# Kernel tuning notes

Measured on AMD Instinct MI355X. Metric: run time of the kernel, lower is better.

## Reference

```python
import jax, jax.numpy as jnp
import numpy as np

B, T, D, H = 2, 1024, 1024, 8  # batch, seq, hidden, num_attention_heads


def setup_inputs() -> dict:
    key = jax.random.key(0)
    ks = jax.random.split(key, 7)
    s = 1.0 / np.sqrt(D)
    return {
        "query": jax.random.normal(ks[0], (B, T, D), jnp.float32),
        "key": jax.random.normal(ks[1], (B, T, D), jnp.float32),
        "value": jax.random.normal(ks[2], (B, T, D), jnp.float32),
        "Wq": jax.random.normal(ks[3], (H, D, D), jnp.float32) * s,
        "Wk": jax.random.normal(ks[4], (H, D, D), jnp.float32) * s,
        "Wv": jax.random.normal(ks[5], (D, D), jnp.float32) * s,
        "Wo": jax.random.normal(ks[6], (D, D), jnp.float32) * s,
    }


def reference(query, key, value, Wq, Wk, Wv, Wo):
    b, t, Dm = query.shape
    h = Wq.shape[0]
    d = Dm // h  # head_dim of the inner split
    # Per-outer-head full linear projections: q_i = query @ Wq[i].T  (nn.Linear, bias=False)
    q = jnp.einsum('btd,ied->ibte', query, Wq)   # (i, b, t, D)
    k = jnp.einsum('bsd,ied->ibse', key, Wk)     # (i, b, s, D)
    v = jnp.einsum('bsd,ed->bse', value, Wv)     # shared values (b, s, D)
    # rearrange 'b t (h d) -> b h t d' per outer head i
    q = q.reshape(h, b, t, h, d).transpose(0, 1, 3, 2, 4)  # (i, b, h, t, d)
    k = k.reshape(h, b, t, h, d).transpose(0, 1, 3, 2, 4)  # (i, b, h, s, d)
    v = v.reshape(b, t, h, d).transpose(0, 2, 1, 3)        # (b, h, s, d)
    scale = jnp.sqrt(jnp.asarray(d, jnp.float32))
    scores = jnp.einsum('ibhtd,ibhsd->ibhts', q, k) / scale
    attn = jax.nn.softmax(scores, axis=-1)                 # (i, b, h, t, s)
    head = jnp.einsum('ibhts,bhsd->ibhtd', attn, v)
    # 'b h t d -> b t (h d)' then stack over i and mean
    head = head.transpose(0, 1, 3, 2, 4).reshape(h, b, t, Dm)
    outputs = jnp.mean(head, axis=0) @ Wo.T                # (b, t, D)
    attention = jnp.mean(attn, axis=0)                     # (b, h, t, s)
    return outputs, attention
```

## Files before the change

kernel.cpp:

```cpp
#include <hip/hip_runtime.h>
#include <hip/hip_bf16.h>

typedef _Float16 f16x8 __attribute__((ext_vector_type(8)));
typedef _Float16 f16x4 __attribute__((ext_vector_type(4)));
typedef float f32x4 __attribute__((ext_vector_type(4)));

typedef __attribute__((address_space(1))) void GV;
typedef __attribute__((address_space(3))) void LV;

__device__ inline void async16(void* lds, const void* g) {
    __builtin_amdgcn_global_load_lds((GV*)g, (LV*)lds, 16, 0, 0);
}

__global__ __launch_bounds__(256) void cast_all(
    const float* __restrict__ q, const float* __restrict__ k, const float* __restrict__ v,
    const float* __restrict__ wq, const float* __restrict__ wk,
    const float* __restrict__ wv, const float* __restrict__ wo, _Float16* __restrict__ ws)
{
    const long M1 = 1048576;
    const long tot = 6291456;
    for (long idx = (long)blockIdx.x * 256 + threadIdx.x; idx < tot;
         idx += (long)gridDim.x * 256) {
        const float* src; long local; long doff;
        if (idx < 1572864) {
            int seg = (int)(idx >> 19);
            src = seg == 0 ? q : (seg == 1 ? k : v);
            local = idx & 524287; doff = (long)seg * 2 * M1;
        } else if (idx < 5767168) {
            int seg = (int)((idx - 1572864) >> 21);
            src = seg == 0 ? wq : wk;
            local = (idx - 1572864) & 2097151; doff = (6 + 8 * (long)seg) * M1;
        } else {
            int seg = (int)((idx - 5767168) >> 18);
            src = seg == 0 ? wv : wo;
            local = (idx - 5767168) & 262143; doff = (22 + (long)seg) * M1;
        }
        float4 val = ((const float4*)src)[local];
        f16x4 o;
        o[0] = (_Float16)val.x; o[1] = (_Float16)val.y;
        o[2] = (_Float16)val.z; o[3] = (_Float16)val.w;
        *(f16x4*)&ws[doff + 4 * local] = o;
    }
}

__global__ __launch_bounds__(256) void transpose_v(const _Float16* __restrict__ in,
                                                   _Float16* __restrict__ out) {
    __shared__ _Float16 tile[64][66];
    int b = blockIdx.z;
    long base = (long)b * 1048576;
    int s0 = blockIdx.x * 64, e0 = blockIdx.y * 64;
    int tc = threadIdx.x & 63, tr = threadIdx.x >> 6;
    #pragma unroll
    for (int rr = 0; rr < 64; rr += 4)
        tile[tr + rr][tc] = in[base + (long)(s0 + tr + rr) * 1024 + e0 + tc];
    __syncthreads();
    #pragma unroll
    for (int rr = 0; rr < 64; rr += 4)
        out[base + (long)(e0 + tr + rr) * 1024 + s0 + tc] = tile[tc][tr + rr];
}

template<int RB, int XS, int OMODE>
__global__ __launch_bounds__(256) void gemm_bt(
    const _Float16* __restrict__ A0, const _Float16* __restrict__ B0, void* __restrict__ C0,
    int K, int lda, int ldb, int ldc,
    int az_div, long sa_hi, long sa_lo, long sb,
    int cz_div, long sc_hi, long sc_lo)
{
    __shared__ _Float16 As[2][RB * 32 * 64];
    __shared__ _Float16 Bs[2][128 * 64];
    int bx, by, bz;
    if (XS) {
        int p = blockIdx.x;
        int xcd = p & 7, s = p >> 3;
        int c, within;
        if (s < 256) { c = xcd + 8 * (s >> 6); within = s & 63; }
        else         { c = 32 + (xcd >> 2); within = (xcd & 3) * 16 + (s - 256); }
        bz = c >> 1;
        by = (c & 1) * 8 + (within >> 3);
        bx = within & 7;
    } else { bx = blockIdx.x; by = blockIdx.y; bz = blockIdx.z; }
    int z = bz;
    const _Float16* A = A0 + (long)(z / az_div) * sa_hi + (long)(z % az_div) * sa_lo;
    const _Float16* B = B0 + (long)z * sb;
    long coff = (long)(z / cz_div) * sc_hi + (long)(z % cz_div) * sc_lo;
    int rowbase = by * (RB * 32), colbase = bx * 128;
    int t = threadIdx.x, wave = t >> 6, lane = t & 63;
    int l15 = lane & 15, lg = lane >> 4;
    int srow = t >> 3, scol = (t & 7) * 8;
    int wm = wave >> 1, wn = wave & 1;
    f32x4 acc[RB][4] = {};
    const int nt = K >> 6;

    #pragma unroll
    for (int ii = 0; ii < RB; ii++) {
        int r = srow + ii * 32;
        async16(&As[0][r * 64 + scol], A + (long)(rowbase + r) * lda + scol);
    }
    #pragma unroll
    for (int ii = 0; ii < 4; ii++) {
        int r = srow + ii * 32;
        async16(&Bs[0][r * 64 + scol], B + (long)(colbase + r) * ldb + scol);
    }

    for (int ts = 0; ts < nt; ts++) {
        __syncthreads();
        if (ts + 1 < nt) {
            int k1 = (ts + 1) << 6;
            int p1 = (ts + 1) & 1;
            #pragma unroll
            for (int ii = 0; ii < RB; ii++) {
                int r = srow + ii * 32;
                async16(&As[p1][r * 64 + scol], A + (long)(rowbase + r) * lda + k1 + scol);
            }
            #pragma unroll
            for (int ii = 0; ii < 4; ii++) {
                int r = srow + ii * 32;
                async16(&Bs[p1][r * 64 + scol], B + (long)(colbase + r) * ldb + k1 + scol);
            }
        }
        int pc = ts & 1;
        #pragma unroll
        for (int ks = 0; ks < 2; ks++) {
            f16x8 af[RB], bfr[4];
            #pragma unroll
            for (int m = 0; m < RB; m++)
                af[m] = *(const f16x8*)&As[pc][(wm * (RB * 16) + m * 16 + l15) * 64 + ks * 32 + lg * 8];
            #pragma unroll
            for (int n = 0; n < 4; n++)
                bfr[n] = *(const f16x8*)&Bs[pc][(wn * 64 + n * 16 + l15) * 64 + ks * 32 + lg * 8];
            #pragma unroll
            for (int m = 0; m < RB; m++)
                #pragma unroll
                for (int n = 0; n < 4; n++)
                    acc[m][n] = __builtin_amdgcn_mfma_f32_16x16x32_f16(af[m], bfr[n], acc[m][n], 0, 0, 0);
        }
    }
    #pragma unroll
    for (int m = 0; m < RB; m++) {
        int row = rowbase + wm * (RB * 16) + m * 16 + lg * 4;
        #pragma unroll
        for (int n = 0; n < 4; n++) {
            int col = colbase + wn * 64 + n * 16 + l15;
            #pragma unroll
            for (int r = 0; r < 4; r++) {
                long idx = coff + (long)(row + r) * ldc + col;
                if (OMODE == 1) ((float*)C0)[idx] = acc[m][n][r];
                else ((_Float16*)C0)[idx] = (_Float16)acc[m][n][r];
            }
        }
    }
}

__global__ __launch_bounds__(256, 2) void attn_fused(
    const _Float16* __restrict__ Qbuf, const _Float16* __restrict__ Kbuf,
    float* __restrict__ attn_out, _Float16* __restrict__ Pbar)
{
    __shared__ _Float16 Kc[4][64 * 128];
    __shared__ float red[4][16];
    int id = blockIdx.x;
    int orig = (id & 7) * 128 + (id >> 3);
    int t0 = (orig & 63) * 16;
    int bh = orig >> 6, h = bh & 7, b = bh >> 3;
    int tid = threadIdx.x, wave = tid >> 6, lane = tid & 63;
    int l15 = lane & 15, lg = lane >> 4;
    int sw = wave;
    int brow = sw * 16 + l15;
    const float scale = 0.088388347648318447f;
    float acc[16][4] = {};

    int srow0 = tid >> 4;
    int scolB = (tid & 15) << 4;
    int gcolB = scolB ^ ((srow0 & 7) << 4);
    int ldsoff = tid * 16;
    const char* pkb = (const char*)(Kbuf + (long)b * 1048576 + h * 128)
                      + (long)srow0 * 2048 + gcolB;
    const char* pq = (const char*)(Qbuf + ((long)(b * 1024 + t0 + l15)) * 1024 + h * 128)
                     + lg * 16;
    int swz = (brow & 7) << 4;
    int rdoff[4];
    #pragma unroll
    for (int kk = 0; kk < 4; kk++)
        rdoff[kk] = brow * 256 + ((kk * 64 + lg * 16) ^ swz);

    #pragma unroll
    for (int mp = 0; mp < 3; mp++) {
        char* lb = (char*)Kc[mp] + ldsoff;
        const char* ps = pkb + (long)mp * 131072;
        #pragma unroll
        for (int j = 0; j < 4; j++)
            async16(lb + j * 4096, ps + (long)j * 32768);
    }

    #pragma unroll 1
    for (int i = 0; i < 8; i++) {
        f16x8 aq[4];
        #pragma unroll
        for (int kk = 0; kk < 4; kk++)
            aq[kk] = *(const f16x8*)(pq + kk * 64);
        pq += 4194304;
        float s[16][4];
        float rs[4] = {0.f, 0.f, 0.f, 0.f};
        #pragma unroll
        for (int c = 0; c < 16; c++) {
            int m = i * 16 + c;
            asm volatile("s_waitcnt vmcnt(8) lgkmcnt(0)" ::: "memory");
            __builtin_amdgcn_s_barrier();
            {
                int n = (m + 3) & 127;
                char* lb = (char*)Kc[(c + 3) & 3] + ldsoff;
                const char* ps = pkb + (long)(n >> 4) * 4194304 + (long)(n & 15) * 131072;
                #pragma unroll
                for (int j = 0; j < 4; j++)
                    async16(lb + j * 4096, ps + (long)j * 32768);
            }
            const char* kc = (const char*)Kc[c & 3];
            f32x4 sv = {0.f, 0.f, 0.f, 0.f};
            #pragma unroll
            for (int kk = 0; kk < 4; kk++) {
                f16x8 bk = *(const f16x8*)(kc + rdoff[kk]);
                sv = __builtin_amdgcn_mfma_f32_16x16x32_f16(aq[kk], bk, sv, 0, 0, 0);
            }
            #pragma unroll
            for (int r = 0; r < 4; r++) {
                float e = __expf(sv[r] * scale);
                s[c][r] = e;
                rs[r] += e;
            }
        }
        #pragma unroll
        for (int off = 1; off < 16; off <<= 1)
            #pragma unroll
            for (int r = 0; r < 4; r++) rs[r] += __shfl_xor(rs[r], off, 64);
        if (l15 == 0) {
            #pragma unroll
            for (int r = 0; r < 4; r++) red[wave][lg * 4 + r] = rs[r];
        }
        asm volatile("s_waitcnt lgkmcnt(0)" ::: "memory");
        __builtin_amdgcn_s_barrier();
        #pragma unroll
        for (int r = 0; r < 4; r++) {
            int row = lg * 4 + r;
            float tot = red[0][row] + red[1][row] + red[2][row] + red[3][row];
            float rinv = 0.125f / tot;
            #pragma unroll
            for (int c = 0; c < 16; c++) acc[c][r] += s[c][r] * rinv;
        }
        asm volatile("s_waitcnt lgkmcnt(0)" ::: "memory");
        __builtin_amdgcn_s_barrier();
    }

    long rbase = ((long)(bh * 1024 + t0)) * 1024;
    #pragma unroll
    for (int c = 0; c < 16; c++) {
        int scol = c * 64 + sw * 16 + l15;
        #pragma unroll
        for (int r = 0; r < 4; r++) {
            long idx = rbase + (long)(lg * 4 + r) * 1024 + scol;
            attn_out[idx] = acc[c][r];
            Pbar[idx] = (_Float16)acc[c][r];
        }
    }
}

extern "C" void kernel_launch(void* const* d_in, const int* in_sizes, int n_in,
                              void* d_out, int out_size, void* d_ws, size_t ws_size,
                              hipStream_t stream) {
    const long M1 = 1048576;
    _Float16* ws = (_Float16*)d_ws;
    _Float16* q16  = ws;
    _Float16* wq16 = ws + 6 * M1;
    _Float16* wo16 = ws + 23 * M1;
    _Float16* Qbuf = ws + 24 * M1;
    _Float16* Vbuf = ws + 56 * M1;
    _Float16* Vt   = ws + 58 * M1;
    _Float16* Pb   = ws + 60 * M1;
    _Float16* Hbar = ws + 76 * M1;
    float* out = (float*)d_out;
    float* attn_out = out + 2 * M1;

    cast_all<<<2048, 256, 0, stream>>>(
        (const float*)d_in[0], (const float*)d_in[1], (const float*)d_in[2],
        (const float*)d_in[3], (const float*)d_in[4], (const float*)d_in[5],
        (const float*)d_in[6], ws);

    gemm_bt<4, 1, 0><<<2176, 256, 0, stream>>>(
        q16, wq16, Qbuf, 1024, 1024, 1024, 1024,
         8, 2 * M1, 0,  M1,
         16, 32 * M1, 2 * M1);
    transpose_v<<<dim3(16, 16, 2), 256, 0, stream>>>(Vbuf, Vt);
    attn_fused<<<1024, 256, 0, stream>>>(Qbuf, Qbuf + 16 * M1, attn_out, Pb);
    gemm_bt<2, 0, 0><<<dim3(1, 16, 16), 256, 0, stream>>>(
        Pb, Vt, Hbar, 1024, 1024, 1024, 1024,
         16, 0, M1,  M1 / 8,
         8, M1, 128);
    gemm_bt<2, 0, 1><<<dim3(8, 32, 1), 256, 0, stream>>>(
        Hbar, wo16, out, 1024, 1024, 1024, 1024,
        1, 0, 0, 0, 1, 0, 0);
}
```

Measured before the change: 304.3 us.

## Restructure GEMM staging into a 4-buffer K=32 pipeline with fragment-ordered LDS

The GEMM main loop moves from a double-buffered K=64 tile to a four-slot ring of K=32 tiles with three stages prefetched, synchronised by explicit vmcnt waits and a raw barrier. LDS is laid out in MFMA fragment order, so each lane reads a contiguous 16-byte slot with no bank conflicts, and launch bounds now request two blocks per CU. The aim is to hide global-load latency and cut LDS bank conflicts. In exchange it uses more LDS per block, relies on hand-tuned waitcnt values, and wraps the prefetch index with nt-1, which assumes nt is a power of two.

```diff
diff --git a/kernel.cpp b/kernel.cpp
--- a/kernel.cpp
+++ b/kernel.cpp
@@ -60,14 +60,15 @@
 }
 
 template<int RB, int XS, int OMODE>
-__global__ __launch_bounds__(256) void gemm_bt(
+__global__ __launch_bounds__(256, 2) void gemm_bt(
     const _Float16* __restrict__ A0, const _Float16* __restrict__ B0, void* __restrict__ C0,
     int K, int lda, int ldb, int ldc,
     int az_div, long sa_hi, long sa_lo, long sb,
     int cz_div, long sc_hi, long sc_lo)
 {
-    __shared__ _Float16 As[2][RB * 32 * 64];
-    __shared__ _Float16 Bs[2][128 * 64];
+    constexpr int ABYTES = RB * 2048;
+    constexpr int BUFB = ABYTES + 8192;
+    __shared__ char Sb[4][BUFB];
     int bx, by, bz;
     if (XS) {
         int p = blockIdx.x;
@@ -86,54 +87,53 @@
     int rowbase = by * (RB * 32), colbase = bx * 128;
     int t = threadIdx.x, wave = t >> 6, lane = t & 63;
     int l15 = lane & 15, lg = lane >> 4;
-    int srow = t >> 3, scol = (t & 7) * 8;
     int wm = wave >> 1, wn = wave & 1;
     f32x4 acc[RB][4] = {};
-    const int nt = K >> 6;
-
-    #pragma unroll
-    for (int ii = 0; ii < RB; ii++) {
-        int r = srow + ii * 32;
-        async16(&As[0][r * 64 + scol], A + (long)(rowbase + r) * lda + scol);
-    }
-    #pragma unroll
-    for (int ii = 0; ii < 4; ii++) {
-        int r = srow + ii * 32;
-        async16(&Bs[0][r * 64 + scol], B + (long)(colbase + r) * ldb + scol);
-    }
+    const int nt = K >> 5;
+
+    int fA0 = t >> 6;
+    int rrS = (t >> 2) & 15;
+    int cbS = (t & 3) * 16;
+    const char* pA = (const char*)(A + (long)(rowbase + fA0 * 16 + rrS) * lda) + cbS;
+    const char* pB = (const char*)(B + (long)(colbase + fA0 * 16 + rrS) * ldb) + cbS;
+    long ldaB = (long)lda * 128;
+    long ldbB = (long)ldb * 128;
+
+    auto STAGE = [&](int buf, int kstep) {
+        long kb = (long)kstep * 64;
+        char* lb = Sb[buf] + t * 16;
+        #pragma unroll
+        for (int j = 0; j < RB / 2; j++)
+            async16(lb + j * 4096, pA + j * ldaB + kb);
+        #pragma unroll
+        for (int j = 0; j < 2; j++)
+            async16(lb + ABYTES + j * 4096, pB + j * ldbB + kb);
+    };
+
+    int lslot = (l15 * 4 + lg) * 16;
+
+    STAGE(0, 0); STAGE(1, 1); STAGE(2, 2);
 
     for (int ts = 0; ts < nt; ts++) {
-        __syncthreads();
-        if (ts + 1 < nt) {
-            int k1 = (ts + 1) << 6;
-            int p1 = (ts + 1) & 1;
-            #pragma unroll
-            for (int ii = 0; ii < RB; ii++) {
-                int r = srow + ii * 32;
-                async16(&As[p1][r * 64 + scol], A + (long)(rowbase + r) * lda + k1 + scol);
-            }
-            #pragma unroll
-            for (int ii = 0; ii < 4; ii++) {
-                int r = srow + ii * 32;
-                async16(&Bs[p1][r * 64 + scol], B + (long)(colbase + r) * ldb + k1 + scol);
-            }
-        }
-        int pc = ts & 1;
-        #pragma unroll
-        for (int ks = 0; ks < 2; ks++) {
-            f16x8 af[RB], bfr[4];
-            #pragma unroll
-            for (int m = 0; m < RB; m++)
-                af[m] = *(const f16x8*)&As[pc][(wm * (RB * 16) + m * 16 + l15) * 64 + ks * 32 + lg * 8];
+        if constexpr (RB == 4)
+            asm volatile("s_waitcnt vmcnt(8) lgkmcnt(0)" ::: "memory");
+        else
+            asm volatile("s_waitcnt vmcnt(6) lgkmcnt(0)" ::: "memory");
+        __builtin_amdgcn_s_barrier();
+        STAGE((ts + 3) & 3, (ts + 3) & (nt - 1));
+        const char* sbuf = Sb[ts & 3];
+        f16x8 af[RB], bfr[4];
+        #pragma unroll
+        for (int m = 0; m < RB; m++)
+            af[m] = *(const f16x8*)(sbuf + (wm * RB + m) * 1024 + lslot);
+        #pragma unroll
+        for (int n = 0; n < 4; n++)
+            bfr[n] = *(const f16x8*)(sbuf + ABYTES + (wn * 4 + n) * 1024 + lslot);
+        #pragma unroll
+        for (int m = 0; m < RB; m++)
             #pragma unroll
             for (int n = 0; n < 4; n++)
-                bfr[n] = *(const f16x8*)&Bs[pc][(wn * 64 + n * 16 + l15) * 64 + ks * 32 + lg * 8];
-            #pragma unroll
-            for (int m = 0; m < RB; m++)
-                #pragma unroll
-                for (int n = 0; n < 4; n++)
-                    acc[m][n] = __builtin_amdgcn_mfma_f32_16x16x32_f16(af[m], bfr[n], acc[m][n], 0, 0, 0);
-        }
+                acc[m][n] = __builtin_amdgcn_mfma_f32_16x16x32_f16(af[m], bfr[n], acc[m][n], 0, 0, 0);
     }
     #pragma unroll
     for (int m = 0; m < RB; m++) {
```

Result: faster. 266.1 us (-12.5%).
